# Kernel optimization log

Hardware: AMD Instinct MI355X
Metric: run time of the kernel (lower is better)

The kernel has to match this reference:

```python
import jax, jax.numpy as jnp
import numpy as np

NUM_SAMPLED = 8192
NUM_TRUE = 1


def setup_inputs() -> dict:
    key = jax.random.key(0)
    k1, k2, k3 = jax.random.split(key, 3)
    B, D, V = 16384, 128, 1000000
    return {
        "movie_id_tensor": jax.random.normal(k1, (B, D), dtype=jnp.float32),
        "target_movie_ids": jax.random.randint(k2, (B, NUM_TRUE), 0, V, dtype=jnp.int64),
        "embedding": jax.random.normal(k3, (V, D), dtype=jnp.float32),
        "bias": jnp.zeros((V,), dtype=jnp.float32),
    }


def _log_uniform_logprob(ids, log_range):
    # log-uniform (Zipf) sampler probability: P(c) = (log(c+2)-log(c+1)) / log(V+1)
    idsf = ids.astype(jnp.float32)
    return jnp.log((jnp.log(idsf + 2.0) - jnp.log(idsf + 1.0)) / log_range)


def reference(movie_id_tensor, target_movie_ids, embedding, bias):
    V, D = embedding.shape
    log_range = jnp.log(jnp.float32(V + 1))
    # --- draw num_sampled candidates from the log-uniform distribution ---
    u = jax.random.uniform(jax.random.key(1), (NUM_SAMPLED,), dtype=jnp.float32)
    sampled = jnp.clip(
        jnp.floor(jnp.exp(u * log_range)).astype(jnp.int32) - 1, 0, V - 1
    )  # [S]
    log_ns = jnp.log(jnp.float32(NUM_SAMPLED))
    # --- gather true-class rows and compute true logits (with logQ correction) ---
    true_w = embedding[target_movie_ids]                  # [B, T, D]
    true_b = bias[target_movie_ids]                       # [B, T]
    true_logits = (
        jnp.einsum("bd,btd->bt", movie_id_tensor, true_w)
        + true_b
        - (log_ns + _log_uniform_logprob(target_movie_ids, log_range))
    )                                                     # [B, T]
    # --- sampled logits (shared candidate set across the batch) ---
    sampled_w = embedding[sampled]                        # [S, D]
    sampled_b = bias[sampled]                             # [S]
    sampled_logits = (
        movie_id_tensor @ sampled_w.T
        + sampled_b
        - (log_ns + _log_uniform_logprob(sampled, log_range))
    )                                                     # [B, S]
    # --- remove accidental hits (sampled id equals a true label) ---
    hit = (sampled[None, None, :] == target_movie_ids[:, :, None]).any(axis=1)  # [B, S]
    sampled_logits = jnp.where(hit, sampled_logits - 1e9, sampled_logits)
    # --- softmax CE with labels = 1/num_true on the true columns ---
    logits = jnp.concatenate([true_logits, sampled_logits], axis=1)  # [B, T+S]
    loss = jax.nn.logsumexp(logits, axis=1) - true_logits.sum(axis=1) / NUM_TRUE
    return loss  # [B]
```

## Files before the change

kernel.cpp:

```cpp
#include <hip/hip_runtime.h>
#include <math.h>

#define BB      16384
#define DD      128
#define VV      1000000
#define NSAMP   8192
#define NT      (NSAMP / 64)

typedef __attribute__((ext_vector_type(8)))  unsigned short u16x8;
typedef __attribute__((ext_vector_type(8)))  __bf16         bf16x8;
typedef __attribute__((ext_vector_type(16))) float          f32x16;

__device__ __forceinline__ unsigned rotl32(unsigned x, unsigned r) {
    return (x << r) | (x >> (32u - r));
}

__device__ __forceinline__ unsigned short bf16r(float v) {
    unsigned b = __builtin_bit_cast(unsigned, v);
    unsigned r = (b + 0x7fffu + ((b >> 16) & 1u)) >> 16;
    return (unsigned short)r;
}

__device__ __forceinline__ float xla_expf(float x) {
#pragma clang fp contract(off)
    float fx = floorf(x * 1.44269504088896341f + 0.5f);
    float tmp = fx * 0.693359375f;
    float z2  = fx * -2.12194440e-4f;
    float r = x - tmp;
    r = r - z2;
    float z = r * r;
    float y = 1.9875691500E-4f;
    y = y * r + 1.3981999507E-3f;
    y = y * r + 8.3334519073E-3f;
    y = y * r + 4.1665795894E-2f;
    y = y * r + 1.6666665459E-1f;
    y = y * r + 5.0000001201E-1f;
    y = y * z + r;
    y = y + 1.0f;
    int n = (int)fx;
    float p2n = __builtin_bit_cast(float, (unsigned)((n + 127) << 23));
    return y * p2n;
}

__device__ __forceinline__ float log_q32(float idf, float logr) {
    float l2 = (float)log((double)(idf + 2.0f));
    float l1 = (float)log((double)(idf + 1.0f));
    float q  = (l2 - l1) / logr;
    return (float)log((double)q);
}

__global__ __launch_bounds__(256) void sample_kernel(
    const unsigned* __restrict__ tgt_raw,
    const float* __restrict__ bias,
    int* __restrict__ ids, float* __restrict__ corr,
    unsigned* __restrict__ flag, float logr, float logns)
{
    if (blockIdx.x == 0) {
        __shared__ unsigned red[256];
        unsigned acc = 0;
        for (int i = threadIdx.x; i < 2048; i += 256) acc |= tgt_raw[2 * i + 1];
        red[threadIdx.x] = acc;
        __syncthreads();
        for (int s = 128; s > 0; s >>= 1) {
            if ((int)threadIdx.x < s) red[threadIdx.x] |= red[threadIdx.x + s];
            __syncthreads();
        }
        if (threadIdx.x == 0) flag[0] = (red[0] == 0u) ? 1u : 0u;
    }

    int i = blockIdx.x * 256 + threadIdx.x;
    if (i >= NSAMP) return;

    const unsigned k0 = 0u, k1 = 1u;
    const unsigned k2 = 0x1BD11BDAu ^ k0 ^ k1;
    unsigned x0 = 0u + k0;
    unsigned x1 = (unsigned)i + k1;
#define TFR(r) { x0 += x1; x1 = rotl32(x1, (r)); x1 ^= x0; }
    TFR(13) TFR(15) TFR(26) TFR(6)   x0 += k1; x1 += k2 + 1u;
    TFR(17) TFR(29) TFR(16) TFR(24)  x0 += k2; x1 += k0 + 2u;
    TFR(13) TFR(15) TFR(26) TFR(6)   x0 += k0; x1 += k1 + 3u;
    TFR(17) TFR(29) TFR(16) TFR(24)  x0 += k1; x1 += k2 + 4u;
    TFR(13) TFR(15) TFR(26) TFR(6)   x0 += k2; x1 += k0 + 5u;
#undef TFR
    unsigned bits = x0 ^ x1;

    unsigned fb = (bits >> 9) | 0x3f800000u;
    float u = __builtin_bit_cast(float, fb) - 1.0f;
    float t = u * logr;
    float ef = xla_expf(t);
    int id = (int)floorf(ef) - 1;
    id = id < 0 ? 0 : (id > VV - 1 ? VV - 1 : id);

    float lp = log_q32((float)id, logr);
    ids[i]  = id;
    corr[i] = bias[id] - (logns + lp);
}

__global__ __launch_bounds__(256) void gather_kernel(
    const float* __restrict__ emb, const int* __restrict__ ids,
    unsigned short* __restrict__ Wh)
{
    int g = blockIdx.x * 256 + threadIdx.x;
    int row   = g >> 4;
    int chunk = g & 15;
    const float4* src = (const float4*)(emb + (size_t)ids[row] * DD + chunk * 8);
    float4 a = src[0], b = src[1];
    uint4 o;
    o.x = (unsigned)bf16r(a.x) | ((unsigned)bf16r(a.y) << 16);
    o.y = (unsigned)bf16r(a.z) | ((unsigned)bf16r(a.w) << 16);
    o.z = (unsigned)bf16r(b.x) | ((unsigned)bf16r(b.y) << 16);
    o.w = (unsigned)bf16r(b.z) | ((unsigned)bf16r(b.w) << 16);
    *(uint4*)(Wh + (size_t)row * DD + chunk * 8) = o;
}

__device__ __forceinline__ int swz(int row, int slot) {
    return row * 256 + ((slot ^ (row & 15)) << 4);
}

__global__ __launch_bounds__(256, 2) void gemm_kernel(
    const float* __restrict__ x, const int* __restrict__ tgt,
    const unsigned* __restrict__ flag,
    const unsigned short* __restrict__ Wh,
    const int* __restrict__ ids, const float* __restrict__ corr,
    float* __restrict__ ps)
{
    __shared__ char lds[32768];

    const int tid  = threadIdx.x;
    const int lane = tid & 63;
    const int wid  = tid >> 6;
    const int wr   = wid >> 1, wc = wid & 1;
    const int half = lane >> 5, ln31 = lane & 31;
    const int m0   = blockIdx.x * 128;
    const int ty0  = blockIdx.y * (NT / 4);

    u16x8 ah[2][8];
    #pragma unroll
    for (int p = 0; p < 2; p++) {
        const float* xr = x + (size_t)(m0 + wr * 64 + p * 32 + ln31) * DD;
        #pragma unroll
        for (int ks = 0; ks < 8; ks++) {
            const float4* pp = (const float4*)(xr + ks * 16 + half * 8);
            float4 f0 = pp[0], f1 = pp[1];
            float v[8] = {f0.x, f0.y, f0.z, f0.w, f1.x, f1.y, f1.z, f1.w};
            u16x8 h;
            #pragma unroll
            for (int j = 0; j < 8; j++) h[j] = bf16r(v[j]);
            ah[p][ks] = h;
        }
    }

    const unsigned is64 = flag[0];
    int t32[2][16];
    #pragma unroll
    for (int p = 0; p < 2; p++)
        #pragma unroll
        for (int i = 0; i < 16; i++) {
            int grow = m0 + wr * 64 + p * 32 + (i & 3) + 8 * (i >> 2) + 4 * half;
            t32[p][i] = is64 ? tgt[2 * grow] : tgt[grow];
        }

    float ss[2][16];
    #pragma unroll
    for (int p = 0; p < 2; p++)
        #pragma unroll
        for (int i = 0; i < 16; i++) ss[p][i] = 0.f;

    const int srow = tid >> 2, s4 = (tid & 3) * 4;
    const int brow = wc * 32 + ln31;

    {
        const uint4* wh = (const uint4*)(Wh + (size_t)(ty0 * 64 + srow) * DD);
        #pragma unroll
        for (int k = 0; k < 4; k++)
            *(uint4*)(lds + swz(srow, s4 + k)) = wh[s4 + k];
    }
    __syncthreads();

    for (int t = 0; t < NT / 4; t++) {
        const int c = t & 1;
        uint4 ph[4];
        const bool pf = (t + 1 < NT / 4);
        if (pf) {
            const uint4* wh = (const uint4*)(Wh + (size_t)((ty0 + t + 1) * 64 + srow) * DD);
            #pragma unroll
            for (int k = 0; k < 4; k++) ph[k] = wh[s4 + k];
        }

        const char* bh_base = lds + c * 16384;
        f32x16 h0, h1;
        #pragma unroll
        for (int q = 0; q < 16; q++) { h0[q] = 0.f; h1[q] = 0.f; }

        #pragma unroll
        for (int ks = 0; ks < 8; ks++) {
            int off = swz(brow, ks * 2 + half);
            bf16x8 bh = __builtin_bit_cast(bf16x8, *(const uint4*)(bh_base + off));
            bf16x8 a0 = __builtin_bit_cast(bf16x8, ah[0][ks]);
            bf16x8 a1 = __builtin_bit_cast(bf16x8, ah[1][ks]);
            h0 = __builtin_amdgcn_mfma_f32_32x32x16_bf16(a0, bh, h0, 0, 0, 0);
            h1 = __builtin_amdgcn_mfma_f32_32x32x16_bf16(a1, bh, h1, 0, 0, 0);
        }

        const int j = (ty0 + t) * 64 + wc * 32 + ln31;
        const float cc = corr[j] - 60.0f;
        const int idj = ids[j];
        #pragma unroll
        for (int i = 0; i < 16; i++) {
            float l0 = h0[i] + cc;
            float l1 = h1[i] + cc;
            ss[0][i] += (idj == t32[0][i]) ? 0.0f : __expf(l0);
            ss[1][i] += (idj == t32[1][i]) ? 0.0f : __expf(l1);
        }

        if (pf) {
            char* db = lds + (c ^ 1) * 16384;
            #pragma unroll
            for (int k = 0; k < 4; k++)
                *(uint4*)(db + swz(srow, s4 + k)) = ph[k];
        }
        __syncthreads();
    }

    #pragma unroll
    for (int p = 0; p < 2; p++)
        #pragma unroll
        for (int i = 0; i < 16; i++) {
            float v = ss[p][i];
            v += __shfl_xor(v, 1);
            v += __shfl_xor(v, 2);
            v += __shfl_xor(v, 4);
            v += __shfl_xor(v, 8);
            v += __shfl_xor(v, 16);
            if (ln31 == 0) {
                int grow = m0 + wr * 64 + p * 32 + (i & 3) + 8 * (i >> 2) + 4 * half;
                ps[(size_t)grow * 8 + blockIdx.y * 2 + wc] = v;
            }
        }
}

__global__ __launch_bounds__(256) void finish_kernel(
    const float* __restrict__ x, const int* __restrict__ tgt,
    const float* __restrict__ emb, const float* __restrict__ bias,
    const unsigned* __restrict__ flag, const float* __restrict__ ps,
    float* __restrict__ out, float logr, float logns)
{
    const int gid = blockIdx.x * 256 + threadIdx.x;
    const int r   = gid >> 4;
    const int l   = gid & 15;
    if (r >= BB) return;

    const int t = flag[0] ? tgt[2 * r] : tgt[r];

    const float4* xr = (const float4*)(x + (size_t)r * DD);
    const float4* wr = (const float4*)(emb + (size_t)t * DD);
    float4 xa = xr[l], xb = xr[l + 16];
    float4 wa = wr[l], wb = wr[l + 16];
    float d = xa.x*wa.x + xa.y*wa.y + xa.z*wa.z + xa.w*wa.w
            + xb.x*wb.x + xb.y*wb.y + xb.z*wb.z + xb.w*wb.w;
    d += __shfl_xor(d, 1);
    d += __shfl_xor(d, 2);
    d += __shfl_xor(d, 4);
    d += __shfl_xor(d, 8);

    if (l == 0) {
        float lp = log_q32((float)t, logr);
        float tl = d + bias[t] - (logns + lp);
        const float* p = ps + (size_t)r * 8;
        float S = ((p[0] + p[1]) + (p[2] + p[3])) + ((p[4] + p[5]) + (p[6] + p[7]));
        out[r] = logf(expf(tl - 60.0f) + S) + 60.0f - tl;
    }
}

extern "C" void kernel_launch(void* const* d_in, const int* in_sizes, int n_in,
                              void* d_out, int out_size, void* d_ws, size_t ws_size,
                              hipStream_t stream)
{
    const float* x    = (const float*)d_in[0];
    const int*   tgt  = (const int*)d_in[1];
    const float* emb  = (const float*)d_in[2];
    const float* bias = (const float*)d_in[3];
    float* out = (float*)d_out;

    char* w = (char*)d_ws;
    int*            ids  = (int*)(w + 0);
    float*          corr = (float*)(w + 32768);
    unsigned*       flag = (unsigned*)(w + 65536);
    unsigned short* Wh   = (unsigned short*)(w + 131072);
    float*          ps   = (float*)(w + 131072 + 2097152);

    const float logr  = (float)log(1000001.0);
    const float logns = (float)log(8192.0);

    sample_kernel<<<dim3(NSAMP / 256), dim3(256), 0, stream>>>(
        (const unsigned*)tgt, bias, ids, corr, flag, logr, logns);
    gather_kernel<<<dim3(NSAMP * 16 / 256), dim3(256), 0, stream>>>(
        emb, ids, Wh);
    gemm_kernel<<<dim3(BB / 128, 4), dim3(256), 0, stream>>>(
        x, tgt, flag, Wh, ids, corr, ps);
    finish_kernel<<<dim3(BB * 16 / 256), dim3(256), 0, stream>>>(
        x, tgt, emb, bias, flag, ps, out, logr, logns);
}
```

Baseline: 80.09 us.

## Pre-convert X to bf16 in prep kernel and use direct global-to-LDS loads

Merges the sampler with a pass that converts the activation matrix to bf16 once, so each GEMM block loads packed bf16 rows instead of converting fp32 on the fly. The W tile double-buffer now uses global_load_lds (direct global-to-LDS) with the swizzle folded into source offsets, which removes register staging and the explicit LDS stores after the MFMA loop. This adds an extra 4MB write and read of Xb plus a larger prep launch.

```diff
diff --git a/kernel.cpp b/kernel.cpp
--- a/kernel.cpp
+++ b/kernel.cpp
@@ -19,6 +19,12 @@
     unsigned b = __builtin_bit_cast(unsigned, v);
     unsigned r = (b + 0x7fffu + ((b >> 16) & 1u)) >> 16;
     return (unsigned short)r;
+}
+
+__device__ __forceinline__ void gload16(const void* g, void* l) {
+    __builtin_amdgcn_global_load_lds(
+        (const __attribute__((address_space(1))) unsigned*)g,
+        (__attribute__((address_space(3))) unsigned*)l, 16, 0, 0);
 }
 
 __device__ __forceinline__ float xla_expf(float x) {
@@ -49,9 +55,10 @@
     return (float)log((double)q);
 }
 
-__global__ __launch_bounds__(256) void sample_kernel(
-    const unsigned* __restrict__ tgt_raw,
+__global__ __launch_bounds__(256) void prep_kernel(
+    const float* __restrict__ x, const unsigned* __restrict__ tgt_raw,
     const float* __restrict__ bias,
+    unsigned short* __restrict__ Xb,
     int* __restrict__ ids, float* __restrict__ corr,
     unsigned* __restrict__ flag, float logr, float logns)
 {
@@ -68,32 +75,45 @@
         if (threadIdx.x == 0) flag[0] = (red[0] == 0u) ? 1u : 0u;
     }
 
-    int i = blockIdx.x * 256 + threadIdx.x;
-    if (i >= NSAMP) return;
-
-    const unsigned k0 = 0u, k1 = 1u;
-    const unsigned k2 = 0x1BD11BDAu ^ k0 ^ k1;
-    unsigned x0 = 0u + k0;
-    unsigned x1 = (unsigned)i + k1;
+    int g = blockIdx.x * 256 + threadIdx.x;
+    {
+        int row = g >> 4, chunk = g & 15;
+        const float4* src = (const float4*)(x + (size_t)row * DD + chunk * 8);
+        float4 a = src[0], b = src[1];
+        uint4 o;
+        o.x = (unsigned)bf16r(a.x) | ((unsigned)bf16r(a.y) << 16);
+        o.y = (unsigned)bf16r(a.z) | ((unsigned)bf16r(a.w) << 16);
+        o.z = (unsigned)bf16r(b.x) | ((unsigned)bf16r(b.y) << 16);
+        o.w = (unsigned)bf16r(b.z) | ((unsigned)bf16r(b.w) << 16);
+        *(uint4*)(Xb + (size_t)row * DD + chunk * 8) = o;
+    }
+
+    if (g < NSAMP) {
+        int i = g;
+        const unsigned k0 = 0u, k1 = 1u;
+        const unsigned k2 = 0x1BD11BDAu ^ k0 ^ k1;
+        unsigned x0 = 0u + k0;
+        unsigned x1 = (unsigned)i + k1;
 #define TFR(r) { x0 += x1; x1 = rotl32(x1, (r)); x1 ^= x0; }
-    TFR(13) TFR(15) TFR(26) TFR(6)   x0 += k1; x1 += k2 + 1u;
-    TFR(17) TFR(29) TFR(16) TFR(24)  x0 += k2; x1 += k0 + 2u;
-    TFR(13) TFR(15) TFR(26) TFR(6)   x0 += k0; x1 += k1 + 3u;
-    TFR(17) TFR(29) TFR(16) TFR(24)  x0 += k1; x1 += k2 + 4u;
-    TFR(13) TFR(15) TFR(26) TFR(6)   x0 += k2; x1 += k0 + 5u;
+        TFR(13) TFR(15) TFR(26) TFR(6)   x0 += k1; x1 += k2 + 1u;
+        TFR(17) TFR(29) TFR(16) TFR(24)  x0 += k2; x1 += k0 + 2u;
+        TFR(13) TFR(15) TFR(26) TFR(6)   x0 += k0; x1 += k1 + 3u;
+        TFR(17) TFR(29) TFR(16) TFR(24)  x0 += k1; x1 += k2 + 4u;
+        TFR(13) TFR(15) TFR(26) TFR(6)   x0 += k2; x1 += k0 + 5u;
 #undef TFR
-    unsigned bits = x0 ^ x1;
-
-    unsigned fb = (bits >> 9) | 0x3f800000u;
-    float u = __builtin_bit_cast(float, fb) - 1.0f;
-    float t = u * logr;
-    float ef = xla_expf(t);
-    int id = (int)floorf(ef) - 1;
-    id = id < 0 ? 0 : (id > VV - 1 ? VV - 1 : id);
-
-    float lp = log_q32((float)id, logr);
-    ids[i]  = id;
-    corr[i] = bias[id] - (logns + lp);
+        unsigned bits = x0 ^ x1;
+
+        unsigned fb = (bits >> 9) | 0x3f800000u;
+        float u = __builtin_bit_cast(float, fb) - 1.0f;
+        float t = u * logr;
+        float ef = xla_expf(t);
+        int id = (int)floorf(ef) - 1;
+        id = id < 0 ? 0 : (id > VV - 1 ? VV - 1 : id);
+
+        float lp = log_q32((float)id, logr);
+        ids[i]  = id;
+        corr[i] = bias[id] - (logns + lp);
+    }
 }
 
 __global__ __launch_bounds__(256) void gather_kernel(
@@ -118,7 +138,7 @@
 }
 
 __global__ __launch_bounds__(256, 2) void gemm_kernel(
-    const float* __restrict__ x, const int* __restrict__ tgt,
+    const unsigned short* __restrict__ Xb, const int* __restrict__ tgt,
     const unsigned* __restrict__ flag,
     const unsigned short* __restrict__ Wh,
     const int* __restrict__ ids, const float* __restrict__ corr,
@@ -137,17 +157,10 @@
     u16x8 ah[2][8];
     #pragma unroll
     for (int p = 0; p < 2; p++) {
-        const float* xr = x + (size_t)(m0 + wr * 64 + p * 32 + ln31) * DD;
-        #pragma unroll
-        for (int ks = 0; ks < 8; ks++) {
-            const float4* pp = (const float4*)(xr + ks * 16 + half * 8);
-            float4 f0 = pp[0], f1 = pp[1];
-            float v[8] = {f0.x, f0.y, f0.z, f0.w, f1.x, f1.y, f1.z, f1.w};
-            u16x8 h;
-            #pragma unroll
-            for (int j = 0; j < 8; j++) h[j] = bf16r(v[j]);
-            ah[p][ks] = h;
-        }
+        const uint4* xr = (const uint4*)(Xb + (size_t)(m0 + wr * 64 + p * 32 + ln31) * DD);
+        #pragma unroll
+        for (int ks = 0; ks < 8; ks++)
+            ah[p][ks] = __builtin_bit_cast(u16x8, xr[ks * 2 + half]);
     }
 
     const unsigned is64 = flag[0];
@@ -166,25 +179,33 @@
         #pragma unroll
         for (int i = 0; i < 16; i++) ss[p][i] = 0.f;
 
-    const int srow = tid >> 2, s4 = (tid & 3) * 4;
+    const int u    = lane & 15;
+    const int rsub = lane >> 4;
+    int srcoff[4], ldsrow[4];
+    #pragma unroll
+    for (int i2 = 0; i2 < 4; i2++) {
+        int row = wid * 16 + i2 * 4 + rsub;
+        srcoff[i2] = row * 256 + ((u ^ (row & 15)) << 4);
+        ldsrow[i2] = (wid * 16 + i2 * 4) * 256;
+    }
     const int brow = wc * 32 + ln31;
 
     {
-        const uint4* wh = (const uint4*)(Wh + (size_t)(ty0 * 64 + srow) * DD);
-        #pragma unroll
-        for (int k = 0; k < 4; k++)
-            *(uint4*)(lds + swz(srow, s4 + k)) = wh[s4 + k];
+        const char* tb = (const char*)Wh + (size_t)(ty0 * 64) * 256;
+        #pragma unroll
+        for (int i2 = 0; i2 < 4; i2++)
+            gload16(tb + srcoff[i2], lds + ldsrow[i2]);
     }
     __syncthreads();
 
     for (int t = 0; t < NT / 4; t++) {
         const int c = t & 1;
-        uint4 ph[4];
-        const bool pf = (t + 1 < NT / 4);
-        if (pf) {
-            const uint4* wh = (const uint4*)(Wh + (size_t)((ty0 + t + 1) * 64 + srow) * DD);
+        if (t + 1 < NT / 4) {
+            const char* tb = (const char*)Wh + (size_t)((ty0 + t + 1) * 64) * 256;
+            char* db = lds + (c ^ 1) * 16384;
             #pragma unroll
-            for (int k = 0; k < 4; k++) ph[k] = wh[s4 + k];
+            for (int i2 = 0; i2 < 4; i2++)
+                gload16(tb + srcoff[i2], db + ldsrow[i2]);
         }
 
         const char* bh_base = lds + c * 16384;
@@ -213,12 +234,6 @@
             ss[1][i] += (idj == t32[1][i]) ? 0.0f : __expf(l1);
         }
 
-        if (pf) {
-            char* db = lds + (c ^ 1) * 16384;
-            #pragma unroll
-            for (int k = 0; k < 4; k++)
-                *(uint4*)(db + swz(srow, s4 + k)) = ph[k];
-        }
         __syncthreads();
     }
 
@@ -286,18 +301,19 @@
     int*            ids  = (int*)(w + 0);
     float*          corr = (float*)(w + 32768);
     unsigned*       flag = (unsigned*)(w + 65536);
-    unsigned short* Wh   = (unsigned short*)(w + 131072);
-    float*          ps   = (float*)(w + 131072 + 2097152);
+    unsigned short* Xb   = (unsigned short*)(w + 131072);
+    unsigned short* Wh   = (unsigned short*)(w + 131072 + 4194304);
+    float*          ps   = (float*)(w + 131072 + 4194304 + 2097152);
 
     const float logr  = (float)log(1000001.0);
     const float logns = (float)log(8192.0);
 
-    sample_kernel<<<dim3(NSAMP / 256), dim3(256), 0, stream>>>(
-        (const unsigned*)tgt, bias, ids, corr, flag, logr, logns);
+    prep_kernel<<<dim3(BB * 16 / 256), dim3(256), 0, stream>>>(
+        x, (const unsigned*)tgt, bias, Xb, ids, corr, flag, logr, logns);
     gather_kernel<<<dim3(NSAMP * 16 / 256), dim3(256), 0, stream>>>(
         emb, ids, Wh);
     gemm_kernel<<<dim3(BB / 128, 4), dim3(256), 0, stream>>>(
-        x, tgt, flag, Wh, ids, corr, ps);
+        Xb, tgt, flag, Wh, ids, corr, ps);
     finish_kernel<<<dim3(BB * 16 / 256), dim3(256), 0, stream>>>(
         x, tgt, emb, bias, flag, ps, out, logr, logns);
 }
```

New measurement: 75.05 us. 1.07x faster.
